# Performance work log

Hardware: AMD Instinct MI355X
Metric: run time of the kernel (lower is better)

Reference implementation:

```python
import jax, jax.numpy as jnp
import numpy as np
import math

NUM_HEADS = 16


def setup_inputs() -> dict:
    key = jax.random.key(0)
    ks = jax.random.split(key, 6)
    L, B, E = 1024, 4, 1024
    D = E // NUM_HEADS
    return {
        "query": jax.random.normal(ks[0], (L, B, E), dtype=jnp.float32),
        "relpos_mat": jax.random.normal(ks[1], (L, D), dtype=jnp.float32),
        "in_proj_weight": jax.random.normal(ks[2], (3 * E, E), dtype=jnp.float32) * 0.02,
        "in_proj_bias": jax.random.normal(ks[3], (3 * E,), dtype=jnp.float32) * 0.02,
        "out_proj_weight": jax.random.normal(ks[4], (E, E), dtype=jnp.float32) * 0.02,
        "out_proj_bias": jax.random.normal(ks[5], (E,), dtype=jnp.float32) * 0.02,
    }


def _skew(qe):
    # qe: (B*H, L, L). Music-Transformer skew trick.
    sz = qe.shape[1]
    mask = jnp.flip(jnp.triu(jnp.ones((sz, sz), dtype=qe.dtype)), axis=0)
    qe = qe * mask
    qe = jnp.pad(qe, ((0, 0), (0, 0), (1, 0)))  # (BH, L, L+1)
    qe = qe.reshape(qe.shape[0], sz + 1, sz)     # (BH, L+1, L)
    return qe[:, 1:, :]                          # (BH, L, L)


def reference(query, relpos_mat, in_proj_weight, in_proj_bias, out_proj_weight, out_proj_bias):
    L, B, E = query.shape
    H = NUM_HEADS
    D = E // H

    # packed QKV projection (self-attention path)
    qkv = query @ in_proj_weight.T + in_proj_bias  # (L, B, 3E)
    q, k, v = jnp.split(qkv, 3, axis=-1)

    def to_bh(x):  # (L, B, E) -> (B*H, L, D)
        return x.reshape(L, B * H, D).transpose(1, 0, 2)

    q = to_bh(q) / math.sqrt(D)
    k = to_bh(k)
    v = to_bh(v)

    attn = jnp.einsum('bld,bmd->blm', q, k)  # (BH, L, L)

    # valid relative embeddings: last L rows
    start = max(0, relpos_mat.shape[0] - L)
    er = relpos_mat[start:, :]               # (L, D)
    qe = jnp.einsum('hld,md->hlm', q, er)    # (BH, L, L)
    srel = _skew(qe)

    attn = jax.nn.softmax(attn + srel, axis=-1)
    out = jnp.einsum('blm,bmd->bld', attn, v)            # (BH, L, D)
    out = out.transpose(1, 0, 2).reshape(L, B, E)         # (L, B, E)
    out = out @ out_proj_weight.T + out_proj_bias
    return out
```

## Files before the change

### kernel.cpp

```cpp
#include <hip/hip_runtime.h>
#include <hip/hip_bf16.h>

#define SL 1024
#define BB 4
#define EE 1024
#define HH 16
#define DD 64
#define BHC 64
#define M1 4096

typedef __bf16 bf16x8 __attribute__((ext_vector_type(8)));
typedef __bf16 bf16x4 __attribute__((ext_vector_type(4)));
typedef float f32x4 __attribute__((ext_vector_type(4)));

typedef __attribute__((address_space(3))) unsigned int lds_u32;
typedef const __attribute__((address_space(1))) unsigned int g_u32;

__device__ __forceinline__ f32x4 mfma16(bf16x8 a, bf16x8 b, f32x4 c) {
    return __builtin_amdgcn_mfma_f32_16x16x32_bf16(a, b, c, 0, 0, 0);
}

#define FR(buf, row, chunk) (*(const bf16x8*)&(buf)[(row) * 64 + (((chunk) ^ ((row) & 7))) * 8])

__global__ __launch_bounds__(256) void f32_to_bf16_k(const float* __restrict__ in,
                                                     __bf16* __restrict__ out, int n) {
    int idx = (blockIdx.x * 256 + threadIdx.x) * 4;
    if (idx >= n) return;
    float4 v = *(const float4*)&in[idx];
    bf16x4 o;
    o[0] = (__bf16)v.x; o[1] = (__bf16)v.y; o[2] = (__bf16)v.z; o[3] = (__bf16)v.w;
    *(bf16x4*)&out[idx] = o;
}

__global__ __launch_bounds__(256) void erflip_k(const float* __restrict__ rel,
                                                __bf16* __restrict__ erf) {
    int idx = blockIdx.x * 256 + threadIdx.x;
    int r = idx >> 6, d = idx & 63;
    erf[idx] = (__bf16)rel[(1023 - r) * 64 + d];
}

#define BMt 128
#define BNt 128
#define BKt 32
__global__ __launch_bounds__(256) void gemm_bt(const __bf16* __restrict__ A,
                                               const __bf16* __restrict__ Bm,
                                               const float* __restrict__ bias,
                                               int M, int N, int K, int mode,
                                               __bf16* __restrict__ q_ws,
                                               __bf16* __restrict__ k_ws,
                                               __bf16* __restrict__ vT_ws,
                                               float* __restrict__ outf) {
    __shared__ __bf16 As[BMt * BKt];
    __shared__ __bf16 Bs[BNt * BKt];
    int tid = threadIdx.x;
    int wave = tid >> 6, lane = tid & 63;
    int quad = lane >> 4, c = lane & 15;
    int ntiles = N / BNt;
    int bx = blockIdx.x % ntiles, by = blockIdx.x / ntiles;
    int m0 = by * BMt, n0 = bx * BNt;
    int wm = (wave >> 1) * 64, wn = (wave & 1) * 64;
    int srow = lane >> 2, scol = (lane & 3) * 8;

    f32x4 acc[4][4] = {};
    for (int k0 = 0; k0 < K; k0 += BKt) {
        __syncthreads();
#pragma unroll
        for (int n = 0; n < 2; ++n) {
            int r0 = 32 * wave + 16 * n;
            const __bf16* ga = &A[(long)(m0 + r0 + srow) * K + k0 + scol];
            const __bf16* gb = &Bm[(long)(n0 + r0 + srow) * K + k0 + scol];
            __builtin_amdgcn_global_load_lds((g_u32*)ga, (lds_u32*)&As[r0 * BKt], 16, 0, 0);
            __builtin_amdgcn_global_load_lds((g_u32*)gb, (lds_u32*)&Bs[r0 * BKt], 16, 0, 0);
        }
        __syncthreads();
        bf16x8 af[4], bfr[4];
#pragma unroll
        for (int t = 0; t < 4; ++t) {
            af[t]  = *(const bf16x8*)&As[(wm + t * 16 + c) * BKt + quad * 8];
            bfr[t] = *(const bf16x8*)&Bs[(wn + t * 16 + c) * BKt + quad * 8];
        }
#pragma unroll
        for (int mt = 0; mt < 4; ++mt)
#pragma unroll
            for (int nt = 0; nt < 4; ++nt)
                acc[mt][nt] = mfma16(af[mt], bfr[nt], acc[mt][nt]);
    }

    if (mode == 1) {
#pragma unroll
        for (int mt = 0; mt < 4; ++mt)
#pragma unroll
            for (int nt = 0; nt < 4; ++nt) {
                int nn = n0 + wn + nt * 16 + c;
                float bv = bias[nn];
#pragma unroll
                for (int i = 0; i < 4; ++i) {
                    int mm = m0 + wm + mt * 16 + quad * 4 + i;
                    outf[(long)mm * N + nn] = acc[mt][nt][i] + bv;
                }
            }
        return;
    }
    __syncthreads();
    __bf16* slab = ((wave < 2) ? As : Bs) + (wave & 1) * 2048;
    int nnb = n0 + wn;
    int which = nnb >> 10;
    int hh = (nnb & 1023) >> 6;
    float scale = (which == 0) ? 0.125f : 1.0f;
#pragma unroll
    for (int mt = 0; mt < 4; ++mt) {
#pragma unroll
        for (int nt = 0; nt < 4; ++nt) {
            float bv = bias[nnb + nt * 16 + c];
#pragma unroll
            for (int i = 0; i < 4; ++i)
                slab[(quad * 4 + i) * 72 + nt * 16 + c] =
                    (__bf16)((acc[mt][nt][i] + bv) * scale);
        }
        if (which < 2) {
            int mm = m0 + wm + mt * 16 + c;
            int l = mm >> 2, bb = mm & 3;
            __bf16* dstp = ((which == 0) ? q_ws : k_ws) +
                           ((long)(bb * 16 + hh) * 1024 + l) * 64;
            bf16x8 t0 = *(const bf16x8*)&slab[c * 72 + quad * 8];
            bf16x8 t1 = *(const bf16x8*)&slab[c * 72 + 32 + quad * 8];
            *(bf16x8*)&dstp[quad * 8] = t0;
            *(bf16x8*)&dstp[32 + quad * 8] = t1;
        } else {
            int d = quad * 16 + c;
            __bf16 tmp[16];
#pragma unroll
            for (int jr = 0; jr < 16; ++jr) tmp[jr] = slab[jr * 72 + d];
            int L0 = (m0 + wm + mt * 16) >> 2;
#pragma unroll
            for (int bs = 0; bs < 4; ++bs) {
                bf16x4 pk;
                pk[0] = tmp[bs]; pk[1] = tmp[4 + bs];
                pk[2] = tmp[8 + bs]; pk[3] = tmp[12 + bs];
                *(bf16x4*)&vT_ws[((long)(bs * 16 + hh) * 64 + d) * 1024 + L0] = pk;
            }
        }
    }
}

#define RST 68
#define PST 72
__global__ __launch_bounds__(256, 2) void attn_kernel(const __bf16* __restrict__ q_ws,
                                                      const __bf16* __restrict__ k_ws,
                                                      const __bf16* __restrict__ vT_ws,
                                                      const __bf16* __restrict__ erf,
                                                      __bf16* __restrict__ O_flat) {
    __shared__ __bf16 Ks[2][4096];
    __shared__ __bf16 Vs[2][4096];
    __shared__ __bf16 Es[2][4096];
    __shared__ __bf16 Ring[4][2 * 16 * RST];
    __shared__ __bf16 Pb[4][16 * PST];

    int tid = threadIdx.x;
    int w = tid >> 6, lane = tid & 63;
    int q = lane >> 4, c = lane & 15;
    int bid = blockIdx.x;
    int x = bid & 7, ii = bid >> 3;
    int bh = x * 8 + (ii >> 4);
    int lt = ii & 15;
    int b = bh >> 4, h = bh & 15;
    int l0w = lt * 64 + w * 16;

    __bf16* RW = Ring[w];
    __bf16* PW = Pb[w];

    const __bf16* qp = q_ws + ((long)bh * 1024 + l0w) * 64;
    bf16x8 qf0 = *(const bf16x8*)&qp[c * 64 + q * 8];
    bf16x8 qf1 = *(const bf16x8*)&qp[c * 64 + 32 + q * 8];

    const __bf16* kbase = k_ws + (long)bh * 65536;
    const __bf16* vbase = vT_ws + (long)bh * 65536;

    int sr[2], sc[2], ldo[2];
#pragma unroll
    for (int n = 0; n < 2; ++n) {
        int sidx = w * 128 + n * 64 + lane;
        sr[n] = sidx >> 3;
        sc[n] = (sidx & 7) ^ (sr[n] & 7);
        ldo[n] = (w * 128 + n * 64) * 8;
    }

#pragma unroll
    for (int n = 0; n < 2; ++n) {
        __builtin_amdgcn_global_load_lds((g_u32*)(kbase + 15 * 4096 + sr[n] * 64 + sc[n] * 8),
                                         (lds_u32*)&Ks[1][ldo[n]], 16, 0, 0);
        __builtin_amdgcn_global_load_lds((g_u32*)(vbase + sr[n] * 1024 + 15 * 64 + sc[n] * 8),
                                         (lds_u32*)&Vs[1][ldo[n]], 16, 0, 0);
    }
    if (lt == 15) {
#pragma unroll
        for (int n = 0; n < 2; ++n)
            __builtin_amdgcn_global_load_lds((g_u32*)(erf + sr[n] * 64 + sc[n] * 8),
                                             (lds_u32*)&Es[1][ldo[n]], 16, 0, 0);
    }
    __syncthreads();

    f32x4 O[4] = {};
    float l_run = 0.f;
    int rowr = l0w + c;

    for (int kt = 15; kt >= 0; --kt) {
        int p = kt & 1;
        if (kt > 0) {
            int pn = p ^ 1;
#pragma unroll
            for (int n = 0; n < 2; ++n) {
                __builtin_amdgcn_global_load_lds(
                    (g_u32*)(kbase + (kt - 1) * 4096 + sr[n] * 64 + sc[n] * 8),
                    (lds_u32*)&Ks[pn][ldo[n]], 16, 0, 0);
                __builtin_amdgcn_global_load_lds(
                    (g_u32*)(vbase + sr[n] * 1024 + (kt - 1) * 64 + sc[n] * 8),
                    (lds_u32*)&Vs[pn][ldo[n]], 16, 0, 0);
            }
            if (kt <= lt + 1) {
                int jn = lt - kt + 1;
#pragma unroll
                for (int n = 0; n < 2; ++n)
                    __builtin_amdgcn_global_load_lds(
                        (g_u32*)(erf + jn * 4096 + sr[n] * 64 + sc[n] * 8),
                        (lds_u32*)&Es[pn][ldo[n]], 16, 0, 0);
            }
        }
        int j = lt - kt;
        if (j >= 0) {
            const __bf16* Ep = Es[p];
            __bf16* rt = RW + (j & 1) * (16 * RST);
#pragma unroll
            for (int s = 0; s < 4; ++s) {
                int row = 16 * s + c;
                f32x4 ar = {0.f, 0.f, 0.f, 0.f};
                ar = mfma16(FR(Ep, row, q), qf0, ar);
                ar = mfma16(FR(Ep, row, 4 + q), qf1, ar);
                bf16x4 pk;
#pragma unroll
                for (int i = 0; i < 4; ++i) pk[i] = (__bf16)ar[i];
                *(bf16x4*)&rt[c * RST + 16 * s + 4 * q] = pk;
            }
        }
        const __bf16* Kp = Ks[p];
        f32x4 S[4];
#pragma unroll
        for (int s = 0; s < 4; ++s) {
            int row = 16 * s + c;
            f32x4 acc = {0.f, 0.f, 0.f, 0.f};
            acc = mfma16(FR(Kp, row, q), qf0, acc);
            acc = mfma16(FR(Kp, row, 4 + q), qf1, acc);
            S[s] = acc;
        }
        if (j >= 0) {
            int rb = rowr - kt * 64 - 4 * q;
#pragma unroll
            for (int s = 0; s < 4; ++s)
#pragma unroll
                for (int i = 0; i < 4; ++i) {
                    int r = rb - 16 * s - i;
                    if (r >= 0)
                        S[s][i] += (float)RW[((r >> 6) & 1) * (16 * RST) + c * RST + (r & 63)];
                }
        }
        float ps[4];
#pragma unroll
        for (int s = 0; s < 4; ++s) {
            float a = __expf(S[s][0]), b2 = __expf(S[s][1]);
            float c2 = __expf(S[s][2]), d2 = __expf(S[s][3]);
            S[s][0] = a; S[s][1] = b2; S[s][2] = c2; S[s][3] = d2;
            ps[s] = (a + b2) + (c2 + d2);
        }
        l_run += (ps[0] + ps[1]) + (ps[2] + ps[3]);
#pragma unroll
        for (int s = 0; s < 4; ++s) {
            bf16x4 pk;
#pragma unroll
            for (int i = 0; i < 4; ++i) pk[i] = (__bf16)S[s][i];
            *(bf16x4*)&PW[c * PST + 16 * s + 4 * q] = pk;
        }
        bf16x8 pa0 = *(const bf16x8*)&PW[c * PST + q * 8];
        bf16x8 pa1 = *(const bf16x8*)&PW[c * PST + 32 + q * 8];
        const __bf16* Vp = Vs[p];
#pragma unroll
        for (int s = 0; s < 4; ++s) {
            int row = 16 * s + c;
            O[s] = mfma16(FR(Vp, row, q), pa0, O[s]);
            O[s] = mfma16(FR(Vp, row, 4 + q), pa1, O[s]);
        }
        __syncthreads();
    }
    float tot = l_run;
    tot += __shfl_xor(tot, 16);
    tot += __shfl_xor(tot, 32);
    float rs = 1.0f / tot;
    long row = (long)(l0w + c) * 4 + b;
#pragma unroll
    for (int s = 0; s < 4; ++s) {
        bf16x4 ov;
#pragma unroll
        for (int i = 0; i < 4; ++i) ov[i] = (__bf16)(O[s][i] * rs);
        *(bf16x4*)&O_flat[row * 1024 + h * 64 + 16 * s + 4 * q] = ov;
    }
}

extern "C" void kernel_launch(void* const* d_in, const int* in_sizes, int n_in,
                              void* d_out, int out_size, void* d_ws, size_t ws_size,
                              hipStream_t stream) {
    const float* query  = (const float*)d_in[0];
    const float* relpos = (const float*)d_in[1];
    const float* w_in   = (const float*)d_in[2];
    const float* b_in   = (const float*)d_in[3];
    const float* w_out  = (const float*)d_in[4];
    const float* b_out  = (const float*)d_in[5];
    float* out = (float*)d_out;

    char* ws = (char*)d_ws;
    size_t off = 0;
    auto alloc = [&](size_t bytes) {
        void* p = ws + off;
        off += (bytes + 255) & ~(size_t)255;
        return p;
    };
    __bf16* qA    = (__bf16*)alloc((size_t)M1 * EE * 2);
    __bf16* winb  = (__bf16*)alloc((size_t)3 * EE * EE * 2);
    __bf16* woutb = (__bf16*)alloc((size_t)EE * EE * 2);
    __bf16* erfp  = (__bf16*)alloc((size_t)SL * DD * 2);
    __bf16* q_ws  = (__bf16*)alloc((size_t)BHC * SL * DD * 2);
    __bf16* k_ws  = (__bf16*)alloc((size_t)BHC * SL * DD * 2);
    __bf16* vT_ws = (__bf16*)alloc((size_t)BHC * SL * DD * 2);
    __bf16* O_flat= (__bf16*)alloc((size_t)M1 * EE * 2);

    f32_to_bf16_k<<<4096, 256, 0, stream>>>(query, qA, M1 * EE);
    f32_to_bf16_k<<<3072, 256, 0, stream>>>(w_in, winb, 3 * EE * EE);
    f32_to_bf16_k<<<1024, 256, 0, stream>>>(w_out, woutb, EE * EE);
    erflip_k<<<256, 256, 0, stream>>>(relpos, erfp);

    gemm_bt<<<(3072 / BNt) * (M1 / BMt), 256, 0, stream>>>(
        qA, winb, b_in, M1, 3072, EE, 0, q_ws, k_ws, vT_ws, nullptr);

    attn_kernel<<<BHC * 16, 256, 0, stream>>>(q_ws, k_ws, vT_ws, erfp, O_flat);

    gemm_bt<<<(1024 / BNt) * (M1 / BMt), 256, 0, stream>>>(
        O_flat, woutb, b_out, M1, 1024, EE, 1, nullptr, nullptr, nullptr, out);
}
```

Before: 232.8 us.

## Process 32 query rows per wave to reuse K/V/E fragments across two row groups

The attention kernel now gives each wave 32 query rows (two 16-row groups), so a block covers 128 rows and the grid shrinks from 1024 to 512 blocks. K, V and relative-embedding fragments are read from LDS once and used for both row groups, which halves LDS traffic per MFMA. V loses its double buffer and is loaded in the same iteration it is used, with an extra barrier added. The P buffer is folded into the ring buffer to fit LDS. The cost is higher register pressure, less overlap of V loads with compute, and fewer blocks to fill the CUs.

Result: faster. 216.1 us (-7.2%).

```diff
diff --git a/kernel.cpp b/kernel.cpp
--- a/kernel.cpp
+++ b/kernel.cpp
@@ -143,35 +143,35 @@
     }
 }
 
-#define RST 68
-#define PST 72
+#define RSTn 72
 __global__ __launch_bounds__(256, 2) void attn_kernel(const __bf16* __restrict__ q_ws,
                                                       const __bf16* __restrict__ k_ws,
                                                       const __bf16* __restrict__ vT_ws,
                                                       const __bf16* __restrict__ erf,
                                                       __bf16* __restrict__ O_flat) {
     __shared__ __bf16 Ks[2][4096];
-    __shared__ __bf16 Vs[2][4096];
+    __shared__ __bf16 Vs[4096];
     __shared__ __bf16 Es[2][4096];
-    __shared__ __bf16 Ring[4][2 * 16 * RST];
-    __shared__ __bf16 Pb[4][16 * PST];
+    __shared__ __bf16 Ring[4][2][32 * RSTn];
 
     int tid = threadIdx.x;
     int w = tid >> 6, lane = tid & 63;
     int q = lane >> 4, c = lane & 15;
     int bid = blockIdx.x;
     int x = bid & 7, ii = bid >> 3;
-    int bh = x * 8 + (ii >> 4);
-    int lt = ii & 15;
+    int bh = x * 8 + (ii >> 3);
+    int blk_l0 = (ii & 7) * 128;
     int b = bh >> 4, h = bh & 15;
-    int l0w = lt * 64 + w * 16;
-
-    __bf16* RW = Ring[w];
-    __bf16* PW = Pb[w];
+    int l0w = blk_l0 + w * 32;
+
+    __bf16* RW = &Ring[w][0][0];
 
     const __bf16* qp = q_ws + ((long)bh * 1024 + l0w) * 64;
-    bf16x8 qf0 = *(const bf16x8*)&qp[c * 64 + q * 8];
-    bf16x8 qf1 = *(const bf16x8*)&qp[c * 64 + 32 + q * 8];
+    bf16x8 qf0[2], qf1[2];
+    qf0[0] = *(const bf16x8*)&qp[c * 64 + q * 8];
+    qf1[0] = *(const bf16x8*)&qp[c * 64 + 32 + q * 8];
+    qf0[1] = *(const bf16x8*)&qp[(16 + c) * 64 + q * 8];
+    qf1[1] = *(const bf16x8*)&qp[(16 + c) * 64 + 32 + q * 8];
 
     const __bf16* kbase = k_ws + (long)bh * 65536;
     const __bf16* vbase = vT_ws + (long)bh * 65536;
@@ -186,121 +186,153 @@
     }
 
 #pragma unroll
-    for (int n = 0; n < 2; ++n) {
+    for (int n = 0; n < 2; ++n)
         __builtin_amdgcn_global_load_lds((g_u32*)(kbase + 15 * 4096 + sr[n] * 64 + sc[n] * 8),
                                          (lds_u32*)&Ks[1][ldo[n]], 16, 0, 0);
-        __builtin_amdgcn_global_load_lds((g_u32*)(vbase + sr[n] * 1024 + 15 * 64 + sc[n] * 8),
-                                         (lds_u32*)&Vs[1][ldo[n]], 16, 0, 0);
-    }
-    if (lt == 15) {
-#pragma unroll
-        for (int n = 0; n < 2; ++n)
-            __builtin_amdgcn_global_load_lds((g_u32*)(erf + sr[n] * 64 + sc[n] * 8),
-                                             (lds_u32*)&Es[1][ldo[n]], 16, 0, 0);
-    }
     __syncthreads();
 
-    f32x4 O[4] = {};
-    float l_run = 0.f;
-    int rowr = l0w + c;
+    f32x4 O[2][4] = {};
+    float l_run[2] = {0.f, 0.f};
 
     for (int kt = 15; kt >= 0; --kt) {
         int p = kt & 1;
         if (kt > 0) {
-            int pn = p ^ 1;
-#pragma unroll
-            for (int n = 0; n < 2; ++n) {
+#pragma unroll
+            for (int n = 0; n < 2; ++n)
                 __builtin_amdgcn_global_load_lds(
                     (g_u32*)(kbase + (kt - 1) * 4096 + sr[n] * 64 + sc[n] * 8),
-                    (lds_u32*)&Ks[pn][ldo[n]], 16, 0, 0);
+                    (lds_u32*)&Ks[p ^ 1][ldo[n]], 16, 0, 0);
+        }
+#pragma unroll
+        for (int n = 0; n < 2; ++n)
+            __builtin_amdgcn_global_load_lds(
+                (g_u32*)(vbase + sr[n] * 1024 + kt * 64 + sc[n] * 8),
+                (lds_u32*)&Vs[ldo[n]], 16, 0, 0);
+        int rmaxB = blk_l0 + 127 - kt * 64;
+        if (rmaxB >= 0) {
+            int tB = rmaxB >> 6;
+#pragma unroll
+            for (int n = 0; n < 2; ++n)
                 __builtin_amdgcn_global_load_lds(
-                    (g_u32*)(vbase + sr[n] * 1024 + (kt - 1) * 64 + sc[n] * 8),
-                    (lds_u32*)&Vs[pn][ldo[n]], 16, 0, 0);
-            }
-            if (kt <= lt + 1) {
-                int jn = lt - kt + 1;
-#pragma unroll
-                for (int n = 0; n < 2; ++n)
-                    __builtin_amdgcn_global_load_lds(
-                        (g_u32*)(erf + jn * 4096 + sr[n] * 64 + sc[n] * 8),
-                        (lds_u32*)&Es[pn][ldo[n]], 16, 0, 0);
-            }
-        }
-        int j = lt - kt;
-        if (j >= 0) {
-            const __bf16* Ep = Es[p];
-            __bf16* rt = RW + (j & 1) * (16 * RST);
-#pragma unroll
-            for (int s = 0; s < 4; ++s) {
-                int row = 16 * s + c;
-                f32x4 ar = {0.f, 0.f, 0.f, 0.f};
-                ar = mfma16(FR(Ep, row, q), qf0, ar);
-                ar = mfma16(FR(Ep, row, 4 + q), qf1, ar);
-                bf16x4 pk;
-#pragma unroll
-                for (int i = 0; i < 4; ++i) pk[i] = (__bf16)ar[i];
-                *(bf16x4*)&rt[c * RST + 16 * s + 4 * q] = pk;
-            }
+                    (g_u32*)(erf + tB * 4096 + sr[n] * 64 + sc[n] * 8),
+                    (lds_u32*)&Es[tB & 1][ldo[n]], 16, 0, 0);
         }
         const __bf16* Kp = Ks[p];
-        f32x4 S[4];
+        bf16x8 ka0[4], ka1[4];
 #pragma unroll
         for (int s = 0; s < 4; ++s) {
             int row = 16 * s + c;
-            f32x4 acc = {0.f, 0.f, 0.f, 0.f};
-            acc = mfma16(FR(Kp, row, q), qf0, acc);
-            acc = mfma16(FR(Kp, row, 4 + q), qf1, acc);
-            S[s] = acc;
-        }
-        if (j >= 0) {
-            int rb = rowr - kt * 64 - 4 * q;
-#pragma unroll
-            for (int s = 0; s < 4; ++s)
-#pragma unroll
-                for (int i = 0; i < 4; ++i) {
-                    int r = rb - 16 * s - i;
-                    if (r >= 0)
-                        S[s][i] += (float)RW[((r >> 6) & 1) * (16 * RST) + c * RST + (r & 63)];
+            ka0[s] = FR(Kp, row, q);
+            ka1[s] = FR(Kp, row, 4 + q);
+        }
+        f32x4 S[2][4];
+#pragma unroll
+        for (int g = 0; g < 2; ++g)
+#pragma unroll
+            for (int s = 0; s < 4; ++s) {
+                f32x4 acc = {0.f, 0.f, 0.f, 0.f};
+                acc = mfma16(ka0[s], qf0[g], acc);
+                acc = mfma16(ka1[s], qf1[g], acc);
+                S[g][s] = acc;
+            }
+        __syncthreads();
+        int rmax = l0w + 31 - kt * 64;
+        int t1 = rmax >> 6;
+        if (rmax >= 0) {
+            const __bf16* Ep = Es[t1 & 1];
+            bf16x8 ea0[4], ea1[4];
+#pragma unroll
+            for (int s = 0; s < 4; ++s) {
+                int row = 16 * s + c;
+                ea0[s] = FR(Ep, row, q);
+                ea1[s] = FR(Ep, row, 4 + q);
+            }
+            __bf16* rt = RW + (t1 & 1) * 2304;
+#pragma unroll
+            for (int g = 0; g < 2; ++g)
+#pragma unroll
+                for (int s = 0; s < 4; ++s) {
+                    f32x4 ar = {0.f, 0.f, 0.f, 0.f};
+                    ar = mfma16(ea0[s], qf0[g], ar);
+                    ar = mfma16(ea1[s], qf1[g], ar);
+                    bf16x4 pk;
+#pragma unroll
+                    for (int i = 0; i < 4; ++i) pk[i] = (__bf16)ar[i];
+                    *(bf16x4*)&rt[(g * 16 + c) * RSTn + 16 * s + 4 * q] = pk;
                 }
-        }
-        float ps[4];
-#pragma unroll
-        for (int s = 0; s < 4; ++s) {
-            float a = __expf(S[s][0]), b2 = __expf(S[s][1]);
-            float c2 = __expf(S[s][2]), d2 = __expf(S[s][3]);
-            S[s][0] = a; S[s][1] = b2; S[s][2] = c2; S[s][3] = d2;
-            ps[s] = (a + b2) + (c2 + d2);
-        }
-        l_run += (ps[0] + ps[1]) + (ps[2] + ps[3]);
-#pragma unroll
-        for (int s = 0; s < 4; ++s) {
-            bf16x4 pk;
-#pragma unroll
-            for (int i = 0; i < 4; ++i) pk[i] = (__bf16)S[s][i];
-            *(bf16x4*)&PW[c * PST + 16 * s + 4 * q] = pk;
-        }
-        bf16x8 pa0 = *(const bf16x8*)&PW[c * PST + q * 8];
-        bf16x8 pa1 = *(const bf16x8*)&PW[c * PST + 32 + q * 8];
-        const __bf16* Vp = Vs[p];
+#pragma unroll
+            for (int g = 0; g < 2; ++g) {
+                int rb = l0w + g * 16 + c - kt * 64 - 4 * q;
+#pragma unroll
+                for (int s = 0; s < 4; ++s)
+#pragma unroll
+                    for (int i = 0; i < 4; ++i) {
+                        int r = rb - 16 * s - i;
+                        if (r >= 0)
+                            S[g][s][i] += (float)RW[((r >> 6) & 1) * 2304 +
+                                                    (g * 16 + c) * RSTn + (r & 63)];
+                    }
+            }
+        }
+        int pslot = (rmax >= 0) ? ((t1 & 1) ^ 1) : 1;
+#pragma unroll
+        for (int g = 0; g < 2; ++g) {
+            float ps[4];
+#pragma unroll
+            for (int s = 0; s < 4; ++s) {
+                float a = __expf(S[g][s][0]), b2 = __expf(S[g][s][1]);
+                float c2 = __expf(S[g][s][2]), d2 = __expf(S[g][s][3]);
+                S[g][s][0] = a; S[g][s][1] = b2; S[g][s][2] = c2; S[g][s][3] = d2;
+                ps[s] = (a + b2) + (c2 + d2);
+            }
+            l_run[g] += (ps[0] + ps[1]) + (ps[2] + ps[3]);
+        }
+        __bf16* PW = RW + pslot * 2304;
+#pragma unroll
+        for (int g = 0; g < 2; ++g)
+#pragma unroll
+            for (int s = 0; s < 4; ++s) {
+                bf16x4 pk;
+#pragma unroll
+                for (int i = 0; i < 4; ++i) pk[i] = (__bf16)S[g][s][i];
+                *(bf16x4*)&PW[(g * 16 + c) * RSTn + 16 * s + 4 * q] = pk;
+            }
+        bf16x8 va0[4], va1[4];
 #pragma unroll
         for (int s = 0; s < 4; ++s) {
             int row = 16 * s + c;
-            O[s] = mfma16(FR(Vp, row, q), pa0, O[s]);
-            O[s] = mfma16(FR(Vp, row, 4 + q), pa1, O[s]);
-        }
+            va0[s] = FR(Vs, row, q);
+            va1[s] = FR(Vs, row, 4 + q);
+        }
+        bf16x8 pa0[2], pa1[2];
+#pragma unroll
+        for (int g = 0; g < 2; ++g) {
+            pa0[g] = *(const bf16x8*)&PW[(g * 16 + c) * RSTn + q * 8];
+            pa1[g] = *(const bf16x8*)&PW[(g * 16 + c) * RSTn + 32 + q * 8];
+        }
+#pragma unroll
+        for (int g = 0; g < 2; ++g)
+#pragma unroll
+            for (int s = 0; s < 4; ++s) {
+                O[g][s] = mfma16(va0[s], pa0[g], O[g][s]);
+                O[g][s] = mfma16(va1[s], pa1[g], O[g][s]);
+            }
         __syncthreads();
     }
-    float tot = l_run;
-    tot += __shfl_xor(tot, 16);
-    tot += __shfl_xor(tot, 32);
-    float rs = 1.0f / tot;
-    long row = (long)(l0w + c) * 4 + b;
-#pragma unroll
-    for (int s = 0; s < 4; ++s) {
-        bf16x4 ov;
-#pragma unroll
-        for (int i = 0; i < 4; ++i) ov[i] = (__bf16)(O[s][i] * rs);
-        *(bf16x4*)&O_flat[row * 1024 + h * 64 + 16 * s + 4 * q] = ov;
+#pragma unroll
+    for (int g = 0; g < 2; ++g) {
+        float tot = l_run[g];
+        tot += __shfl_xor(tot, 16);
+        tot += __shfl_xor(tot, 32);
+        float rs = 1.0f / tot;
+        long row = (long)(l0w + g * 16 + c) * 4 + b;
+#pragma unroll
+        for (int s = 0; s < 4; ++s) {
+            bf16x4 ov;
+#pragma unroll
+            for (int i = 0; i < 4; ++i) ov[i] = (__bf16)(O[g][s][i] * rs);
+            *(bf16x4*)&O_flat[row * 1024 + h * 64 + 16 * s + 4 * q] = ov;
+        }
     }
 }
 
@@ -339,7 +371,7 @@
     gemm_bt<<<(3072 / BNt) * (M1 / BMt), 256, 0, stream>>>(
         qA, winb, b_in, M1, 3072, EE, 0, q_ws, k_ws, vT_ws, nullptr);
 
-    attn_kernel<<<BHC * 16, 256, 0, stream>>>(q_ws, k_ws, vT_ws, erfp, O_flat);
+    attn_kernel<<<512, 256, 0, stream>>>(q_ws, k_ws, vT_ws, erfp, O_flat);
 
     gemm_bt<<<(1024 / BNt) * (M1 / BMt), 256, 0, stream>>>(
         O_flat, woutb, b_out, M1, 1024, EE, 1, nullptr, nullptr, nullptr, out);
```
